# Kernel tuning notes

Measured on AMD Instinct MI355X. Metric: run time of the kernel, lower is better.

The kernel has to match this reference:

```python
import jax, jax.numpy as jnp
import numpy as np

# MediaPipe hand landmark indices
THUMB_MCP, THUMB_IP, THUMB_TIP = 2, 3, 4
INDEX_MCP, INDEX_PIP, INDEX_TIP = 5, 6, 8
MIDDLE_MCP, MIDDLE_PIP, MIDDLE_TIP = 9, 10, 12
RING_MCP, RING_PIP, RING_TIP = 13, 14, 16
PINKY_MCP, PINKY_PIP, PINKY_TIP = 17, 18, 20
JOINT_TRIPLETS = [(0,1,2),(1,2,3),(2,3,4),(0,5,6),(5,6,7),(6,7,8),(0,9,10),(9,10,11),(10,11,12),(0,13,14),(13,14,15),(14,15,16),(0,17,18),(17,18,19),(18,19,20)]
SPREAD_MCPS = [5, 9, 13, 17]
NOSE, CHIN, FOREHEAD = 42, 43, 44
L_SH, R_SH, L_EL, R_EL = 45, 46, 47, 48
U_LIP, L_LIP = 49, 50


def _dist(a, b):
    return jnp.sqrt(((a - b) ** 2).sum(-1) + 1e-6)


def _norm(v):
    return jnp.sqrt((v * v).sum(-1))


def _acos(c):
    return jnp.arccos(jnp.clip(c, -1.0 + 1e-6, 1.0 - 1e-6))


def _cdiff(x):
    # central difference along time axis=1 with edge replication
    v = (x[:, 2:] - x[:, :-2]) * 0.5
    return jnp.concatenate([v[:, :1], v, v[:, -1:]], axis=1)


def geo_features(xyz, face_mask, body_mask):
    # xyz: [B, T, N, 3] -> [B, T, 114]
    d = _dist
    p = lambda i: xyz[:, :, i]            # [B,T,3]
    feats = []

    # --- per-hand tip/curl features (12 per hand) ---
    for base in (0, 21):
        tips = [d(p(base + THUMB_TIP), p(base + INDEX_TIP)),
                d(p(base + INDEX_TIP), p(base + MIDDLE_TIP)),
                d(p(base + MIDDLE_TIP), p(base + RING_TIP)),
                d(p(base + RING_TIP), p(base + PINKY_TIP)),
                d(p(base + THUMB_TIP), p(base + PINKY_TIP))]
        curls = [d(p(base + THUMB_MCP), p(base + THUMB_TIP)) / (d(p(base + THUMB_MCP), p(base + THUMB_IP)) + 1e-4),
                 d(p(base + INDEX_MCP), p(base + INDEX_TIP)) / (d(p(base + INDEX_MCP), p(base + INDEX_PIP)) + 1e-4),
                 d(p(base + MIDDLE_MCP), p(base + MIDDLE_TIP)) / (d(p(base + MIDDLE_MCP), p(base + MIDDLE_PIP)) + 1e-4),
                 d(p(base + RING_MCP), p(base + RING_TIP)) / (d(p(base + RING_MCP), p(base + RING_PIP)) + 1e-4),
                 d(p(base + PINKY_MCP), p(base + PINKY_TIP)) / (d(p(base + PINKY_MCP), p(base + PINKY_PIP)) + 1e-4)]
        cross = xyz[:, :, base + INDEX_TIP, 0] - xyz[:, :, base + MIDDLE_TIP, 0]
        d_ti = d(p(base + THUMB_TIP), p(base + INDEX_MCP))
        feats += tips + curls + [cross, d_ti]

    # --- face distances (10), gated by face_mask ---
    fg = face_mask[:, :, 0, 0]
    face = [d(p(0), p(NOSE)), d(p(0), p(CHIN)), d(p(0), p(FOREHEAD)),
            d(p(21), p(NOSE)), d(p(21), p(CHIN)), d(p(21), p(FOREHEAD)),
            d(p(INDEX_TIP), p(NOSE)), d(p(INDEX_TIP), p(FOREHEAD)),
            d(p(21 + INDEX_TIP), p(NOSE)), d(p(21 + INDEX_TIP), p(FOREHEAD))]
    feats += [f * fg for f in face]

    # --- joint angles (30), vectorized gather over 2 hands x 15 triplets ---
    P = np.array([b + t[0] for b in (0, 21) for t in JOINT_TRIPLETS])
    J = np.array([b + t[1] for b in (0, 21) for t in JOINT_TRIPLETS])
    C = np.array([b + t[2] for b in (0, 21) for t in JOINT_TRIPLETS])
    v1 = xyz[:, :, P] - xyz[:, :, J]      # [B,T,30,3]
    v2 = xyz[:, :, C] - xyz[:, :, J]
    ang = _acos((v1 * v2).sum(-1) / (_norm(v1) * _norm(v2) + 1e-6))  # [B,T,30]
    feats += [ang[..., i] for i in range(ang.shape[-1])]

    # --- palm normals (6) ---
    for base in (0, 21):
        w = p(base)
        n = jnp.cross(p(base + 5) - w, p(base + 17) - w)
        n = n / (_norm(n)[..., None] + 1e-6)
        feats += [n[..., i] for i in range(3)]

    # --- finger spread angles (6) ---
    for base in (0, 21):
        w = p(base)
        for i in range(len(SPREAD_MCPS) - 1):
            v1 = p(base + SPREAD_MCPS[i]) - w
            v2 = p(base + SPREAD_MCPS[i + 1]) - w
            feats.append(_acos((v1 * v2).sum(-1) / (_norm(v1) * _norm(v2) + 1e-6)))

    # --- palm orientation vs up/forward (4) ---
    up = jnp.array([0.0, 1.0, 0.0], dtype=xyz.dtype)
    fwd = jnp.array([0.0, 0.0, 1.0], dtype=xyz.dtype)
    for base in (0, 21):
        w = p(base)
        n = jnp.cross(p(base + 5) - w, p(base + 17) - w)
        n = n / (_norm(n)[..., None] + 1e-6)
        feats += [(n * up).sum(-1), (n * fwd).sum(-1)]

    # --- wrist trajectory direction (6) ---
    for base in (0, 21):
        vel = _cdiff(p(base))
        vd = vel / jnp.maximum(_norm(vel)[..., None], 1e-6)
        feats += [vd[..., i] for i in range(3)]

    # --- trajectory curvature (2) ---
    for base in (0, 21):
        vel = _cdiff(p(base))
        vn = vel / (_norm(vel)[..., None] + 1e-6)
        dot = (vn[:, :-1] * vn[:, 1:]).sum(-1)
        feats.append(jnp.pad(_acos(dot), ((0, 0), (0, 1))))

    # --- inter-hand (3) ---
    feats.append(d(p(0), p(21)))
    rel = p(21) - p(0)
    rn = rel / (_norm(rel)[..., None] + 1e-6)
    feats += [rn[..., 0], rn[..., 1]]

    # --- approach velocity to nose (2) ---
    for base in (0, 21):
        dist = _norm(p(base) - p(NOSE))
        feats.append(_cdiff(dist[..., None])[..., 0])

    # --- finger x-crossings (4) ---
    for base in (0, 21):
        feats.append(xyz[:, :, base + INDEX_TIP, 0] - xyz[:, :, base + MIDDLE_TIP, 0])
        feats.append(xyz[:, :, base + MIDDLE_TIP, 0] - xyz[:, :, base + RING_TIP, 0])

    # --- hand motion symmetry (1) ---
    lv, rv = _cdiff(p(0)), _cdiff(p(21))
    ld = lv / (_norm(lv)[..., None] + 1e-6)
    rd = rv / (_norm(rv)[..., None] + 1e-6)
    feats.append((ld * rd).sum(-1))

    # --- speed (2) and acceleration (2) ---
    for base in (0, 21):
        feats.append(_norm(_cdiff(p(base))))
    for base in (0, 21):
        feats.append(_norm(_cdiff(_cdiff(p(base)))))

    # --- hand contact (1) ---
    hd = _norm(p(0) - p(21))
    feats.append(jax.nn.sigmoid(5.0 * (0.05 - hd)))

    # --- body-relative features (11), gated by body_mask ---
    bg = body_mask[:, :, 0, 0]
    l_sh, r_sh = p(L_SH), p(R_SH)
    sh_mid = (l_sh + r_sh) * 0.5
    sh_w = d(l_sh, r_sh)
    body = []
    for base in (0, 21):
        w = p(base)
        body.append((w[:, :, 1] - sh_mid[:, :, 1]) / (sh_w + 1e-6))
        body.append((w[:, :, 0] - sh_mid[:, :, 0]) / (sh_w + 1e-6))
        body.append(d(w, l_sh if base == 0 else r_sh))
        body.append(d(w, p(L_EL if base == 0 else R_EL)))
    body.append(sh_w)
    mouth = (p(U_LIP) + p(L_LIP)) * 0.5
    body.append(d(p(0), mouth))
    body.append(d(p(21), mouth))
    feats += [f * bg for f in body]

    return jnp.stack(feats, axis=-1)  # [B,T,114]


def setup_inputs() -> dict:
    key = jax.random.key(0)
    B, T, N = 256, 512, 51
    xyz = jax.random.normal(key, (B, T, N, 3), dtype=jnp.float32)
    face_mask = jnp.ones((B, T, 1, 1), dtype=jnp.float32)
    body_mask = jnp.ones((B, T, 1, 1), dtype=jnp.float32)
    return {"xyz": xyz, "face_mask": face_mask, "body_mask": body_mask}


def reference(xyz, face_mask, body_mask):
    return geo_features(xyz, face_mask, body_mask)
```

## Files before the change

### kernel.cpp

```cpp
#include <hip/hip_runtime.h>
#include <math.h>


#define NF   114
#define NC   153
#define TILE 64
#define HSTR 65
#define FSTR 33
#define HALO 4
#define HN   (TILE + 2 * HALO)

struct V3 { float x, y, z; };

__device__ __forceinline__ V3 operator-(V3 a, V3 b) { return {a.x - b.x, a.y - b.y, a.z - b.z}; }
__device__ __forceinline__ V3 operator+(V3 a, V3 b) { return {a.x + b.x, a.y + b.y, a.z + b.z}; }
__device__ __forceinline__ V3 operator*(V3 a, float s) { return {a.x * s, a.y * s, a.z * s}; }
__device__ __forceinline__ float dot3(V3 a, V3 b) { return a.x * b.x + a.y * b.y + a.z * b.z; }
__device__ __forceinline__ V3 cross3(V3 a, V3 b) {
    return {a.y * b.z - a.z * b.y, a.z * b.x - a.x * b.z, a.x * b.y - a.y * b.x};
}
__device__ __forceinline__ float norm3(V3 a) { return sqrtf(dot3(a, a)); }
__device__ __forceinline__ float dist3(V3 a, V3 b) { V3 d = a - b; return sqrtf(dot3(d, d) + 1e-6f); }
__device__ __forceinline__ float acosc(float c) {
    c = fminf(fmaxf(c, -1.0f + 1e-6f), 1.0f - 1e-6f);
    return acosf(c);
}

__device__ __forceinline__ void bmap(int tt, int T, int& ta, int& tb) {
    if (tt == 0)          { ta = 0;      tb = 2;     }
    else if (tt == T - 1) { ta = T - 3;  tb = T - 1; }
    else                  { ta = tt - 1; tb = tt + 1; }
}

__global__ __launch_bounds__(64, 2) void geo_fused(
    const float* __restrict__ xyz,
    const float* __restrict__ fmask,
    const float* __restrict__ bmask,
    float* __restrict__ out,
    int T)
{
    __shared__ float Sh[TILE * HSTR];
    __shared__ float Hb[HN * 9];

    const int tid = threadIdx.x;
    const int tilesPerRow = T / TILE;
    const int b   = blockIdx.x / tilesPerRow;
    const int t0  = (blockIdx.x - b * tilesPerRow) * TILE;
    const int t   = t0 + tid;
    const int bT0 = b * T;
    const int idx = bT0 + t;

    const float fg = fmask[idx];
    const float bg = bmask[idx];

    float F[NF];

    {
        const int offs[9] = {0, 1, 2, 63, 64, 65, 126, 127, 128};
        #pragma unroll
        for (int rr = 0; rr < 2; ++rr) {
            int j = tid + (rr << 6);
            if (j < HN) {
                int th = t0 - HALO + j;
                th = th < 0 ? 0 : (th > T - 1 ? T - 1 : th);
                const float* rec = xyz + (size_t)(bT0 + th) * NC;
                #pragma unroll
                for (int c = 0; c < 9; ++c)
                    Hb[j * 9 + c] = rec[offs[c]];
            }
        }
    }

    {
        const float* gb = xyz + (size_t)(bT0 + t0) * NC;
        #pragma unroll
        for (int k = 0; k < TILE; ++k)
            Sh[k * HSTR + tid] = gb[(size_t)k * NC + tid];
    }
    __syncthreads();

    {
        auto HP = [&](int cb, int th) -> V3 {
            int j = (th - t0 + HALO) * 9 + cb;
            return V3{Hb[j], Hb[j + 1], Hb[j + 2]};
        };
        auto wvel = [&](int cb, int tt) -> V3 {
            int ta, tb; bmap(tt, T, ta, tb);
            return (HP(cb, tb) - HP(cb, ta)) * 0.5f;
        };
        auto wacc = [&](int cb, int tt) -> V3 {
            int ta, tb; bmap(tt, T, ta, tb);
            return (wvel(cb, tb) - wvel(cb, ta)) * 0.5f;
        };

        V3 velW0 = wvel(0, t), velW1 = wvel(3, t);

        {
            float inv = 1.0f / fmaxf(norm3(velW0), 1e-6f);
            F[80] = velW0.x * inv; F[81] = velW0.y * inv; F[82] = velW0.z * inv;
        }
        {
            float inv = 1.0f / fmaxf(norm3(velW1), 1e-6f);
            F[83] = velW1.x * inv; F[84] = velW1.y * inv; F[85] = velW1.z * inv;
        }
        #pragma unroll
        for (int h = 0; h < 2; ++h) {
            float val = 0.0f;
            if (t < T - 1) {
                V3 v0 = (h == 0) ? velW0 : velW1;
                V3 v1 = wvel(h * 3, t + 1);
                V3 a  = v0 * (1.0f / (norm3(v0) + 1e-6f));
                V3 c  = v1 * (1.0f / (norm3(v1) + 1e-6f));
                val = acosc(dot3(a, c));
            }
            F[86 + h] = val;
        }
        V3 p0h = HP(0, t), p21h = HP(3, t);
        F[88] = dist3(p0h, p21h);
        {
            V3 rel = p21h - p0h;
            float inv = 1.0f / (norm3(rel) + 1e-6f);
            F[89] = rel.x * inv; F[90] = rel.y * inv;
        }
        #pragma unroll
        for (int h = 0; h < 2; ++h) {
            int ta, tb; bmap(t, T, ta, tb);
            float da = norm3(HP(h * 3, ta) - HP(6, ta));
            float db = norm3(HP(h * 3, tb) - HP(6, tb));
            F[91 + h] = (db - da) * 0.5f;
        }
        {
            V3 ldv = velW0 * (1.0f / (norm3(velW0) + 1e-6f));
            V3 rdv = velW1 * (1.0f / (norm3(velW1) + 1e-6f));
            F[97] = dot3(ldv, rdv);
        }
        F[98] = norm3(velW0);
        F[99] = norm3(velW1);
        F[100] = norm3(wacc(0, t));
        F[101] = norm3(wacc(3, t));
        {
            float hd = norm3(p0h - p21h);
            F[102] = 1.0f / (1.0f + expf(-5.0f * (0.05f - hd)));
        }
    }

    V3 p0, p21, itip0, itip1;
    constexpr int TRI[15][3] = {
        {0, 1, 2},   {1, 2, 3},   {2, 3, 4},
        {0, 5, 6},   {5, 6, 7},   {6, 7, 8},
        {0, 9, 10},  {9, 10, 11}, {10, 11, 12},
        {0, 13, 14}, {13, 14, 15},{14, 15, 16},
        {0, 17, 18}, {17, 18, 19},{18, 19, 20}};

    #pragma unroll
    for (int h = 0; h < 2; ++h) {
        if (h == 1) {
            __syncthreads();
            const float* gb = xyz + (size_t)(bT0 + t0) * NC + 63;
            #pragma unroll
            for (int k = 0; k < TILE; ++k)
                Sh[k * HSTR + tid] = gb[(size_t)k * NC + tid];
            __syncthreads();
        }

        const float* R = Sh + tid * HSTR;
        auto PL = [&](int lm) -> V3 {
            int c = 3 * lm;
            return V3{R[c], R[c + 1], R[c + 2]};
        };

        {
            V3 t_tip = PL(4),  i_tip = PL(8),  m_tip = PL(12);
            V3 r_tip = PL(16), p_tip = PL(20);
            int oa = h * 12;
            F[oa + 0] = dist3(t_tip, i_tip);
            F[oa + 1] = dist3(i_tip, m_tip);
            F[oa + 2] = dist3(m_tip, r_tip);
            F[oa + 3] = dist3(r_tip, p_tip);
            F[oa + 4] = dist3(t_tip, p_tip);
            V3 tm = PL(2),  tj = PL(3);
            F[oa + 5] = dist3(tm, t_tip) / (dist3(tm, tj) + 1e-4f);
            V3 im = PL(5),  ij = PL(6);
            F[oa + 6] = dist3(im, i_tip) / (dist3(im, ij) + 1e-4f);
            V3 mm = PL(9),  mj = PL(10);
            F[oa + 7] = dist3(mm, m_tip) / (dist3(mm, mj) + 1e-4f);
            V3 rm = PL(13), rj = PL(14);
            F[oa + 8] = dist3(rm, r_tip) / (dist3(rm, rj) + 1e-4f);
            V3 pm = PL(17), pj = PL(18);
            F[oa + 9] = dist3(pm, p_tip) / (dist3(pm, pj) + 1e-4f);
            F[oa + 10] = i_tip.x - m_tip.x;
            F[oa + 11] = dist3(t_tip, im);
            F[93 + 2 * h + 0] = i_tip.x - m_tip.x;
            F[93 + 2 * h + 1] = m_tip.x - r_tip.x;
            if (h == 0) itip0 = i_tip; else itip1 = i_tip;
        }
        #pragma unroll
        for (int i = 0; i < 15; ++i) {
            V3 pj = PL(TRI[i][1]);
            V3 v1 = PL(TRI[i][0]) - pj;
            V3 v2 = PL(TRI[i][2]) - pj;
            F[34 + h * 15 + i] = acosc(dot3(v1, v2) / (norm3(v1) * norm3(v2) + 1e-6f));
        }
        {
            V3 w = PL(0);
            V3 n = cross3(PL(5) - w, PL(17) - w);
            float inv = 1.0f / (norm3(n) + 1e-6f);
            n = n * inv;
            F[64 + 3 * h + 0] = n.x;
            F[64 + 3 * h + 1] = n.y;
            F[64 + 3 * h + 2] = n.z;
            F[76 + 2 * h + 0] = n.y;
            F[76 + 2 * h + 1] = n.z;
            V3 v5  = PL(5)  - w;
            V3 v9  = PL(9)  - w;
            V3 v13 = PL(13) - w;
            V3 v17 = PL(17) - w;
            F[70 + 3 * h + 0] = acosc(dot3(v5,  v9)  / (norm3(v5)  * norm3(v9)  + 1e-6f));
            F[70 + 3 * h + 1] = acosc(dot3(v9,  v13) / (norm3(v9)  * norm3(v13) + 1e-6f));
            F[70 + 3 * h + 2] = acosc(dot3(v13, v17) / (norm3(v13) * norm3(v17) + 1e-6f));
            if (h == 0) p0 = w; else p21 = w;
        }
    }

    __syncthreads();
    {
        const float* gf = xyz + (size_t)(bT0 + t0) * NC + 121;
        #pragma unroll
        for (int k = 0; k < 32; ++k) {
            int rec = 2 * k + (tid >> 5);
            int c   = tid & 31;
            Sh[rec * FSTR + c] = gf[(size_t)rec * NC + c];
        }
    }
    __syncthreads();
    {
        const float* R2 = Sh + tid * FSTR;
        auto FL = [&](int k) -> V3 {
            int c = 5 + 3 * k;
            return V3{R2[c], R2[c + 1], R2[c + 2]};
        };
        V3 nose = FL(0), chin = FL(1), fore = FL(2);
        F[24] = dist3(p0,  nose) * fg;
        F[25] = dist3(p0,  chin) * fg;
        F[26] = dist3(p0,  fore) * fg;
        F[27] = dist3(p21, nose) * fg;
        F[28] = dist3(p21, chin) * fg;
        F[29] = dist3(p21, fore) * fg;
        F[30] = dist3(itip0, nose) * fg;
        F[31] = dist3(itip0, fore) * fg;
        F[32] = dist3(itip1, nose) * fg;
        F[33] = dist3(itip1, fore) * fg;
        V3 lsh = FL(3), rsh = FL(4);
        V3 shmid = (lsh + rsh) * 0.5f;
        float shw = dist3(lsh, rsh);
        float invw = 1.0f / (shw + 1e-6f);
        F[103] = (p0.y  - shmid.y) * invw * bg;
        F[104] = (p0.x  - shmid.x) * invw * bg;
        F[105] = dist3(p0, lsh) * bg;
        F[106] = dist3(p0, FL(5)) * bg;
        F[107] = (p21.y - shmid.y) * invw * bg;
        F[108] = (p21.x - shmid.x) * invw * bg;
        F[109] = dist3(p21, rsh) * bg;
        F[110] = dist3(p21, FL(6)) * bg;
        F[111] = shw * bg;
        V3 mouth = (FL(7) + FL(8)) * 0.5f;
        F[112] = dist3(p0,  mouth) * bg;
        F[113] = dist3(p21, mouth) * bg;
    }

    float* o = out + (size_t)idx * NF;
    #pragma unroll
    for (int f = 0; f < NF; f += 2) {
        float2 v; v.x = F[f]; v.y = F[f + 1];
        *reinterpret_cast<float2*>(o + f) = v;
    }
}

__constant__ int c_TRI[15][3] = {
    {0, 1, 2},   {1, 2, 3},   {2, 3, 4},
    {0, 5, 6},   {5, 6, 7},   {6, 7, 8},
    {0, 9, 10},  {9, 10, 11}, {10, 11, 12},
    {0, 13, 14}, {13, 14, 15},{14, 15, 16},
    {0, 17, 18}, {17, 18, 19},{18, 19, 20}};

__global__ __launch_bounds__(256) void geo_direct(
    const float* __restrict__ xyz,
    const float* __restrict__ fmask,
    const float* __restrict__ bmask,
    float* __restrict__ out,
    int BT, int T)
{
    int idx = blockIdx.x * blockDim.x + threadIdx.x;
    if (idx >= BT) return;
    int b = idx / T;
    int t = idx - b * T;
    int bT0 = b * T;

    auto ldp = [&](int tt, int lm) -> V3 {
        const float* p = xyz + ((size_t)(bT0 + tt) * 51 + (size_t)lm) * 3;
        return V3{p[0], p[1], p[2]};
    };
    auto P = [&](int lm) -> V3 { return ldp(t, lm); };
    auto velAt = [&](int lm, int tt) -> V3 {
        int ta, tb; bmap(tt, T, ta, tb);
        return (ldp(tb, lm) - ldp(ta, lm)) * 0.5f;
    };
    auto accAt = [&](int lm, int tt) -> V3 {
        int ta, tb; bmap(tt, T, ta, tb);
        return (velAt(lm, tb) - velAt(lm, ta)) * 0.5f;
    };

    float fg = fmask[idx];
    float bg = bmask[idx];
    float* o = out + (size_t)idx * NF;

    for (int h = 0; h < 2; ++h) {
        int base = h * 21;
        V3 t_tip = P(base + 4),  i_tip = P(base + 8),  m_tip = P(base + 12);
        V3 r_tip = P(base + 16), p_tip = P(base + 20);
        float* oa = o + h * 12;
        oa[0] = dist3(t_tip, i_tip);
        oa[1] = dist3(i_tip, m_tip);
        oa[2] = dist3(m_tip, r_tip);
        oa[3] = dist3(r_tip, p_tip);
        oa[4] = dist3(t_tip, p_tip);
        V3 tm = P(base + 2),  tj = P(base + 3);
        oa[5] = dist3(tm, t_tip) / (dist3(tm, tj) + 1e-4f);
        V3 im = P(base + 5),  ij = P(base + 6);
        oa[6] = dist3(im, i_tip) / (dist3(im, ij) + 1e-4f);
        V3 mm = P(base + 9),  mj = P(base + 10);
        oa[7] = dist3(mm, m_tip) / (dist3(mm, mj) + 1e-4f);
        V3 rm = P(base + 13), rj = P(base + 14);
        oa[8] = dist3(rm, r_tip) / (dist3(rm, rj) + 1e-4f);
        V3 pm = P(base + 17), pj = P(base + 18);
        oa[9] = dist3(pm, p_tip) / (dist3(pm, pj) + 1e-4f);
        oa[10] = i_tip.x - m_tip.x;
        oa[11] = dist3(t_tip, im);
    }

    V3 p0 = P(0), p21 = P(21);
    V3 nose = P(42), chin = P(43), fore = P(44);
    V3 itip0 = P(8), itip1 = P(29);
    o[24] = dist3(p0, nose) * fg;
    o[25] = dist3(p0, chin) * fg;
    o[26] = dist3(p0, fore) * fg;
    o[27] = dist3(p21, nose) * fg;
    o[28] = dist3(p21, chin) * fg;
    o[29] = dist3(p21, fore) * fg;
    o[30] = dist3(itip0, nose) * fg;
    o[31] = dist3(itip0, fore) * fg;
    o[32] = dist3(itip1, nose) * fg;
    o[33] = dist3(itip1, fore) * fg;

    for (int h = 0; h < 2; ++h) {
        int base = h * 21;
        for (int i = 0; i < 15; ++i) {
            V3 pj = P(base + c_TRI[i][1]);
            V3 v1 = P(base + c_TRI[i][0]) - pj;
            V3 v2 = P(base + c_TRI[i][2]) - pj;
            o[34 + h * 15 + i] = acosc(dot3(v1, v2) / (norm3(v1) * norm3(v2) + 1e-6f));
        }
    }

    V3 nrm[2];
    for (int h = 0; h < 2; ++h) {
        int base = h * 21;
        V3 w = (h == 0) ? p0 : p21;
        V3 n = cross3(P(base + 5) - w, P(base + 17) - w);
        float inv = 1.0f / (norm3(n) + 1e-6f);
        n = n * inv;
        nrm[h] = n;
        o[64 + 3 * h + 0] = n.x;
        o[64 + 3 * h + 1] = n.y;
        o[64 + 3 * h + 2] = n.z;
    }

    for (int h = 0; h < 2; ++h) {
        int base = h * 21;
        V3 w = (h == 0) ? p0 : p21;
        V3 v5  = P(base + 5)  - w;
        V3 v9  = P(base + 9)  - w;
        V3 v13 = P(base + 13) - w;
        V3 v17 = P(base + 17) - w;
        o[70 + 3 * h + 0] = acosc(dot3(v5,  v9)  / (norm3(v5)  * norm3(v9)  + 1e-6f));
        o[70 + 3 * h + 1] = acosc(dot3(v9,  v13) / (norm3(v9)  * norm3(v13) + 1e-6f));
        o[70 + 3 * h + 2] = acosc(dot3(v13, v17) / (norm3(v13) * norm3(v17) + 1e-6f));
    }

    for (int h = 0; h < 2; ++h) {
        o[76 + 2 * h + 0] = nrm[h].y;
        o[76 + 2 * h + 1] = nrm[h].z;
    }

    V3 velW[2];
    for (int h = 0; h < 2; ++h) {
        V3 v = velAt(h * 21, t);
        velW[h] = v;
        float inv = 1.0f / fmaxf(norm3(v), 1e-6f);
        o[80 + 3 * h + 0] = v.x * inv;
        o[80 + 3 * h + 1] = v.y * inv;
        o[80 + 3 * h + 2] = v.z * inv;
    }

    for (int h = 0; h < 2; ++h) {
        float val = 0.0f;
        if (t < T - 1) {
            V3 v0 = velW[h];
            V3 v1 = velAt(h * 21, t + 1);
            V3 a = v0 * (1.0f / (norm3(v0) + 1e-6f));
            V3 c = v1 * (1.0f / (norm3(v1) + 1e-6f));
            val = acosc(dot3(a, c));
        }
        o[86 + h] = val;
    }

    o[88] = dist3(p0, p21);
    {
        V3 rel = p21 - p0;
        float inv = 1.0f / (norm3(rel) + 1e-6f);
        o[89] = rel.x * inv;
        o[90] = rel.y * inv;
    }

    for (int h = 0; h < 2; ++h) {
        int lm = h * 21;
        int ta, tb; bmap(t, T, ta, tb);
        float da = norm3(ldp(ta, lm) - ldp(ta, 42));
        float db = norm3(ldp(tb, lm) - ldp(tb, 42));
        o[91 + h] = (db - da) * 0.5f;
    }

    for (int h = 0; h < 2; ++h) {
        int base = h * 21;
        float ix = P(base + 8).x, mx = P(base + 12).x, rx = P(base + 16).x;
        o[93 + 2 * h + 0] = ix - mx;
        o[93 + 2 * h + 1] = mx - rx;
    }

    {
        V3 ldv = velW[0] * (1.0f / (norm3(velW[0]) + 1e-6f));
        V3 rdv = velW[1] * (1.0f / (norm3(velW[1]) + 1e-6f));
        o[97] = dot3(ldv, rdv);
    }

    o[98] = norm3(velW[0]);
    o[99] = norm3(velW[1]);
    o[100] = norm3(accAt(0, t));
    o[101] = norm3(accAt(21, t));

    {
        float hd = norm3(p0 - p21);
        o[102] = 1.0f / (1.0f + expf(-5.0f * (0.05f - hd)));
    }

    {
        V3 lsh = P(45), rsh = P(46);
        V3 shmid = (lsh + rsh) * 0.5f;
        float shw = dist3(lsh, rsh);
        float invw = 1.0f / (shw + 1e-6f);
        o[103] = (p0.y - shmid.y) * invw * bg;
        o[104] = (p0.x - shmid.x) * invw * bg;
        o[105] = dist3(p0, lsh) * bg;
        o[106] = dist3(p0, P(47)) * bg;
        o[107] = (p21.y - shmid.y) * invw * bg;
        o[108] = (p21.x - shmid.x) * invw * bg;
        o[109] = dist3(p21, rsh) * bg;
        o[110] = dist3(p21, P(48)) * bg;
        o[111] = shw * bg;
        V3 mouth = (P(49) + P(50)) * 0.5f;
        o[112] = dist3(p0, mouth) * bg;
        o[113] = dist3(p21, mouth) * bg;
    }
}

extern "C" void kernel_launch(void* const* d_in, const int* in_sizes, int n_in,
                              void* d_out, int out_size, void* d_ws, size_t ws_size,
                              hipStream_t stream) {
    const float* xyz   = (const float*)d_in[0];
    const float* fmask = (const float*)d_in[1];
    const float* bmask = (const float*)d_in[2];
    float* out = (float*)d_out;

    const int BT = in_sizes[1];
    const int T  = 512;

    if (T % TILE == 0 && BT % T == 0 && T >= 3 * TILE) {
        geo_fused<<<BT / TILE, TILE, 0, stream>>>(xyz, fmask, bmask, out, T);
    } else {
        const int threads = 256;
        geo_direct<<<(BT + threads - 1) / threads, threads, 0, stream>>>(
            xyz, fmask, bmask, out, BT, T);
    }
}
```

Baseline: 164.8 us.

## Use async global-to-LDS loads, double-buffer hand tiles, and fast math intrinsics

Both hand tiles are fetched up front into two separate LDS buffers using global_load_lds DMA. This removes the mid-kernel reload and one barrier. The face/body tile load is issued between the two hand computations so it can overlap with compute. Divisions, sqrt and exp are replaced with hardware rcp/sqrt/__expf, and acosf with a polynomial approximation. Precision drops, LDS use per block doubles, and the DMA path issued by only 32 threads may depend on wave-wide LDS addressing semantics.

```diff
diff --git a/kernel.cpp b/kernel.cpp
--- a/kernel.cpp
+++ b/kernel.cpp
@@ -10,6 +10,26 @@
 #define HALO 4
 #define HN   (TILE + 2 * HALO)
 
+#if defined(__has_builtin)
+#if __has_builtin(__builtin_amdgcn_global_load_lds)
+#define USE_DMA 1
+#endif
+#endif
+#ifndef USE_DMA
+#define USE_DMA 0
+#endif
+
+typedef const __attribute__((address_space(1))) void gas_t;
+typedef __attribute__((address_space(3))) void las_t;
+
+__device__ __forceinline__ void dma4(const float* g, float* lds) {
+#if USE_DMA
+    __builtin_amdgcn_global_load_lds((gas_t*)g, (las_t*)lds, 4, 0, 0);
+#else
+    lds[threadIdx.x & 63] = *g;
+#endif
+}
+
 struct V3 { float x, y, z; };
 
 __device__ __forceinline__ V3 operator-(V3 a, V3 b) { return {a.x - b.x, a.y - b.y, a.z - b.z}; }
@@ -19,11 +39,19 @@
 __device__ __forceinline__ V3 cross3(V3 a, V3 b) {
     return {a.y * b.z - a.z * b.y, a.z * b.x - a.x * b.z, a.x * b.y - a.y * b.x};
 }
-__device__ __forceinline__ float norm3(V3 a) { return sqrtf(dot3(a, a)); }
-__device__ __forceinline__ float dist3(V3 a, V3 b) { V3 d = a - b; return sqrtf(dot3(d, d) + 1e-6f); }
+
+__device__ __forceinline__ float fsqrt(float x) { return __builtin_amdgcn_sqrtf(x); }
+__device__ __forceinline__ float frcp(float x)  { return __builtin_amdgcn_rcpf(x); }
+
+__device__ __forceinline__ float norm3(V3 a) { return fsqrt(dot3(a, a)); }
+__device__ __forceinline__ float dist3(V3 a, V3 b) { V3 d = a - b; return fsqrt(dot3(d, d) + 1e-6f); }
+
 __device__ __forceinline__ float acosc(float c) {
     c = fminf(fmaxf(c, -1.0f + 1e-6f), 1.0f - 1e-6f);
-    return acosf(c);
+    float ax = fabsf(c);
+    float r = fsqrt(1.0f - ax) *
+              (1.5707288f + ax * (-0.2121144f + ax * (0.0742610f - 0.0187293f * ax)));
+    return c < 0.0f ? 3.14159265358979f - r : r;
 }
 
 __device__ __forceinline__ void bmap(int tt, int T, int& ta, int& tb) {
@@ -39,7 +67,8 @@
     float* __restrict__ out,
     int T)
 {
-    __shared__ float Sh[TILE * HSTR];
+    __shared__ float Sh0[TILE * HSTR];
+    __shared__ float Sh1[TILE * HSTR];
     __shared__ float Hb[HN * 9];
 
     const int tid = threadIdx.x;
@@ -50,10 +79,14 @@
     const int bT0 = b * T;
     const int idx = bT0 + t;
 
-    const float fg = fmask[idx];
-    const float bg = bmask[idx];
-
-    float F[NF];
+    const float* gb = xyz + (size_t)(bT0 + t0) * NC;
+
+    #pragma unroll
+    for (int k = 0; k < TILE; ++k)
+        dma4(gb + (size_t)k * NC + tid, Sh0 + k * HSTR);
+    #pragma unroll
+    for (int k = 0; k < TILE; ++k)
+        dma4(gb + (size_t)k * NC + 63 + tid, Sh1 + k * HSTR);
 
     {
         const int offs[9] = {0, 1, 2, 63, 64, 65, 126, 127, 128};
@@ -71,13 +104,12 @@
         }
     }
 
-    {
-        const float* gb = xyz + (size_t)(bT0 + t0) * NC;
-        #pragma unroll
-        for (int k = 0; k < TILE; ++k)
-            Sh[k * HSTR + tid] = gb[(size_t)k * NC + tid];
-    }
+    const float fg = fmask[idx];
+    const float bg = bmask[idx];
+
     __syncthreads();
+
+    float F[NF];
 
     {
         auto HP = [&](int cb, int th) -> V3 {
@@ -96,11 +128,11 @@
         V3 velW0 = wvel(0, t), velW1 = wvel(3, t);
 
         {
-            float inv = 1.0f / fmaxf(norm3(velW0), 1e-6f);
+            float inv = frcp(fmaxf(norm3(velW0), 1e-6f));
             F[80] = velW0.x * inv; F[81] = velW0.y * inv; F[82] = velW0.z * inv;
         }
         {
-            float inv = 1.0f / fmaxf(norm3(velW1), 1e-6f);
+            float inv = frcp(fmaxf(norm3(velW1), 1e-6f));
             F[83] = velW1.x * inv; F[84] = velW1.y * inv; F[85] = velW1.z * inv;
         }
         #pragma unroll
@@ -109,8 +141,8 @@
             if (t < T - 1) {
                 V3 v0 = (h == 0) ? velW0 : velW1;
                 V3 v1 = wvel(h * 3, t + 1);
-                V3 a  = v0 * (1.0f / (norm3(v0) + 1e-6f));
-                V3 c  = v1 * (1.0f / (norm3(v1) + 1e-6f));
+                V3 a  = v0 * frcp(norm3(v0) + 1e-6f);
+                V3 c  = v1 * frcp(norm3(v1) + 1e-6f);
                 val = acosc(dot3(a, c));
             }
             F[86 + h] = val;
@@ -119,7 +151,7 @@
         F[88] = dist3(p0h, p21h);
         {
             V3 rel = p21h - p0h;
-            float inv = 1.0f / (norm3(rel) + 1e-6f);
+            float inv = frcp(norm3(rel) + 1e-6f);
             F[89] = rel.x * inv; F[90] = rel.y * inv;
         }
         #pragma unroll
@@ -130,8 +162,8 @@
             F[91 + h] = (db - da) * 0.5f;
         }
         {
-            V3 ldv = velW0 * (1.0f / (norm3(velW0) + 1e-6f));
-            V3 rdv = velW1 * (1.0f / (norm3(velW1) + 1e-6f));
+            V3 ldv = velW0 * frcp(norm3(velW0) + 1e-6f);
+            V3 rdv = velW1 * frcp(norm3(velW1) + 1e-6f);
             F[97] = dot3(ldv, rdv);
         }
         F[98] = norm3(velW0);
@@ -140,101 +172,91 @@
         F[101] = norm3(wacc(3, t));
         {
             float hd = norm3(p0h - p21h);
-            F[102] = 1.0f / (1.0f + expf(-5.0f * (0.05f - hd)));
+            F[102] = frcp(1.0f + __expf(-5.0f * (0.05f - hd)));
         }
     }
 
     V3 p0, p21, itip0, itip1;
-    constexpr int TRI[15][3] = {
-        {0, 1, 2},   {1, 2, 3},   {2, 3, 4},
-        {0, 5, 6},   {5, 6, 7},   {6, 7, 8},
-        {0, 9, 10},  {9, 10, 11}, {10, 11, 12},
-        {0, 13, 14}, {13, 14, 15},{14, 15, 16},
-        {0, 17, 18}, {17, 18, 19},{18, 19, 20}};
-
-    #pragma unroll
-    for (int h = 0; h < 2; ++h) {
-        if (h == 1) {
-            __syncthreads();
-            const float* gb = xyz + (size_t)(bT0 + t0) * NC + 63;
-            #pragma unroll
-            for (int k = 0; k < TILE; ++k)
-                Sh[k * HSTR + tid] = gb[(size_t)k * NC + tid];
-            __syncthreads();
-        }
-
-        const float* R = Sh + tid * HSTR;
+
+    auto handFeats = [&](const float* R, int h, V3& wrist, V3& itip) {
+        constexpr int TRI[15][3] = {
+            {0, 1, 2},   {1, 2, 3},   {2, 3, 4},
+            {0, 5, 6},   {5, 6, 7},   {6, 7, 8},
+            {0, 9, 10},  {9, 10, 11}, {10, 11, 12},
+            {0, 13, 14}, {13, 14, 15},{14, 15, 16},
+            {0, 17, 18}, {17, 18, 19},{18, 19, 20}};
         auto PL = [&](int lm) -> V3 {
             int c = 3 * lm;
             return V3{R[c], R[c + 1], R[c + 2]};
         };
-
-        {
-            V3 t_tip = PL(4),  i_tip = PL(8),  m_tip = PL(12);
-            V3 r_tip = PL(16), p_tip = PL(20);
-            int oa = h * 12;
-            F[oa + 0] = dist3(t_tip, i_tip);
-            F[oa + 1] = dist3(i_tip, m_tip);
-            F[oa + 2] = dist3(m_tip, r_tip);
-            F[oa + 3] = dist3(r_tip, p_tip);
-            F[oa + 4] = dist3(t_tip, p_tip);
-            V3 tm = PL(2),  tj = PL(3);
-            F[oa + 5] = dist3(tm, t_tip) / (dist3(tm, tj) + 1e-4f);
-            V3 im = PL(5),  ij = PL(6);
-            F[oa + 6] = dist3(im, i_tip) / (dist3(im, ij) + 1e-4f);
-            V3 mm = PL(9),  mj = PL(10);
-            F[oa + 7] = dist3(mm, m_tip) / (dist3(mm, mj) + 1e-4f);
-            V3 rm = PL(13), rj = PL(14);
-            F[oa + 8] = dist3(rm, r_tip) / (dist3(rm, rj) + 1e-4f);
-            V3 pm = PL(17), pj = PL(18);
-            F[oa + 9] = dist3(pm, p_tip) / (dist3(pm, pj) + 1e-4f);
-            F[oa + 10] = i_tip.x - m_tip.x;
-            F[oa + 11] = dist3(t_tip, im);
-            F[93 + 2 * h + 0] = i_tip.x - m_tip.x;
-            F[93 + 2 * h + 1] = m_tip.x - r_tip.x;
-            if (h == 0) itip0 = i_tip; else itip1 = i_tip;
-        }
+        V3 t_tip = PL(4),  i_tip = PL(8),  m_tip = PL(12);
+        V3 r_tip = PL(16), p_tip = PL(20);
+        int oa = h * 12;
+        F[oa + 0] = dist3(t_tip, i_tip);
+        F[oa + 1] = dist3(i_tip, m_tip);
+        F[oa + 2] = dist3(m_tip, r_tip);
+        F[oa + 3] = dist3(r_tip, p_tip);
+        F[oa + 4] = dist3(t_tip, p_tip);
+        V3 tm = PL(2),  tj = PL(3);
+        F[oa + 5] = dist3(tm, t_tip) * frcp(dist3(tm, tj) + 1e-4f);
+        V3 im = PL(5),  ij = PL(6);
+        F[oa + 6] = dist3(im, i_tip) * frcp(dist3(im, ij) + 1e-4f);
+        V3 mm = PL(9),  mj = PL(10);
+        F[oa + 7] = dist3(mm, m_tip) * frcp(dist3(mm, mj) + 1e-4f);
+        V3 rm = PL(13), rj = PL(14);
+        F[oa + 8] = dist3(rm, r_tip) * frcp(dist3(rm, rj) + 1e-4f);
+        V3 pm = PL(17), pj = PL(18);
+        F[oa + 9] = dist3(pm, p_tip) * frcp(dist3(pm, pj) + 1e-4f);
+        F[oa + 10] = i_tip.x - m_tip.x;
+        F[oa + 11] = dist3(t_tip, im);
+        F[93 + 2 * h + 0] = i_tip.x - m_tip.x;
+        F[93 + 2 * h + 1] = m_tip.x - r_tip.x;
+        itip = i_tip;
         #pragma unroll
         for (int i = 0; i < 15; ++i) {
-            V3 pj = PL(TRI[i][1]);
-            V3 v1 = PL(TRI[i][0]) - pj;
-            V3 v2 = PL(TRI[i][2]) - pj;
-            F[34 + h * 15 + i] = acosc(dot3(v1, v2) / (norm3(v1) * norm3(v2) + 1e-6f));
-        }
-        {
-            V3 w = PL(0);
-            V3 n = cross3(PL(5) - w, PL(17) - w);
-            float inv = 1.0f / (norm3(n) + 1e-6f);
-            n = n * inv;
-            F[64 + 3 * h + 0] = n.x;
-            F[64 + 3 * h + 1] = n.y;
-            F[64 + 3 * h + 2] = n.z;
-            F[76 + 2 * h + 0] = n.y;
-            F[76 + 2 * h + 1] = n.z;
-            V3 v5  = PL(5)  - w;
-            V3 v9  = PL(9)  - w;
-            V3 v13 = PL(13) - w;
-            V3 v17 = PL(17) - w;
-            F[70 + 3 * h + 0] = acosc(dot3(v5,  v9)  / (norm3(v5)  * norm3(v9)  + 1e-6f));
-            F[70 + 3 * h + 1] = acosc(dot3(v9,  v13) / (norm3(v9)  * norm3(v13) + 1e-6f));
-            F[70 + 3 * h + 2] = acosc(dot3(v13, v17) / (norm3(v13) * norm3(v17) + 1e-6f));
-            if (h == 0) p0 = w; else p21 = w;
-        }
-    }
+            V3 pjv = PL(TRI[i][1]);
+            V3 v1 = PL(TRI[i][0]) - pjv;
+            V3 v2 = PL(TRI[i][2]) - pjv;
+            F[34 + h * 15 + i] = acosc(dot3(v1, v2) * frcp(norm3(v1) * norm3(v2) + 1e-6f));
+        }
+        V3 w = PL(0);
+        V3 n = cross3(PL(5) - w, PL(17) - w);
+        float inv = frcp(norm3(n) + 1e-6f);
+        n = n * inv;
+        F[64 + 3 * h + 0] = n.x;
+        F[64 + 3 * h + 1] = n.y;
+        F[64 + 3 * h + 2] = n.z;
+        F[76 + 2 * h + 0] = n.y;
+        F[76 + 2 * h + 1] = n.z;
+        V3 v5  = PL(5)  - w;
+        V3 v9  = PL(9)  - w;
+        V3 v13 = PL(13) - w;
+        V3 v17 = PL(17) - w;
+        F[70 + 3 * h + 0] = acosc(dot3(v5,  v9)  * frcp(norm3(v5)  * norm3(v9)  + 1e-6f));
+        F[70 + 3 * h + 1] = acosc(dot3(v9,  v13) * frcp(norm3(v9)  * norm3(v13) + 1e-6f));
+        F[70 + 3 * h + 2] = acosc(dot3(v13, v17) * frcp(norm3(v13) * norm3(v17) + 1e-6f));
+        wrist = w;
+    };
+
+    handFeats(Sh0 + tid * HSTR, 0, p0, itip0);
 
     __syncthreads();
     {
-        const float* gf = xyz + (size_t)(bT0 + t0) * NC + 121;
-        #pragma unroll
-        for (int k = 0; k < 32; ++k) {
-            int rec = 2 * k + (tid >> 5);
-            int c   = tid & 31;
-            Sh[rec * FSTR + c] = gf[(size_t)rec * NC + c];
-        }
-    }
+        const float* gf = gb + 121;
+        float* Sf = Sh0;
+        if (tid < 32) {
+            #pragma unroll
+            for (int k = 0; k < TILE; ++k)
+                dma4(gf + (size_t)k * NC + tid, Sf + k * FSTR);
+        }
+    }
+
+    handFeats(Sh1 + tid * HSTR, 1, p21, itip1);
+
     __syncthreads();
-    {
-        const float* R2 = Sh + tid * FSTR;
+
+    {
+        const float* R2 = Sh0 + tid * FSTR;
         auto FL = [&](int k) -> V3 {
             int c = 5 + 3 * k;
             return V3{R2[c], R2[c + 1], R2[c + 2]};
@@ -253,7 +275,7 @@
         V3 lsh = FL(3), rsh = FL(4);
         V3 shmid = (lsh + rsh) * 0.5f;
         float shw = dist3(lsh, rsh);
-        float invw = 1.0f / (shw + 1e-6f);
+        float invw = frcp(shw + 1e-6f);
         F[103] = (p0.y  - shmid.y) * invw * bg;
         F[104] = (p0.x  - shmid.x) * invw * bg;
         F[105] = dist3(p0, lsh) * bg;
```

New measurement: 162.3 us. No clear change (-1.5%).
